# Kernel tuning notes

Hardware: AMD Instinct MI355X
Metric: run time of the kernel (lower is better)

The kernel has to match this reference:

```python
import jax, jax.numpy as jnp
import numpy as np

B, P, K, G_PER, F_IN, H, NECK = 16, 512, 32, 8, 59, 128, 512
N = B * P
E = N * K
G = N // G_PER
EPS = 1e-5


def setup_inputs() -> dict:
    rng = np.random.default_rng(0)
    f32 = lambda a: jnp.asarray(a, jnp.float32)
    x = f32(rng.standard_normal((N, F_IN)))
    pos = f32(rng.standard_normal((N, 3)) * 8.0)
    nrm = rng.standard_normal((N, 3))
    normal = f32(nrm / np.linalg.norm(nrm, axis=1, keepdims=True))
    # synthetic radius-graph edges: K neighbors per node within its own graph, incl. self edge
    nbr = rng.integers(0, P, size=(N, K))
    nbr[:, 0] = np.arange(N) % P  # self edge guarantees every dst segment is non-empty
    starts = np.repeat(np.arange(B) * P, P)
    src = jnp.asarray((starts[:, None] + nbr).reshape(-1), jnp.int32)
    dst = jnp.asarray(np.repeat(np.arange(N), K), jnp.int32)
    # raw (unnormalized but consecutive-run) residue labels, relabeled inside reference
    pool_batch = jnp.asarray(np.repeat(np.arange(G) * 3 + 7, G_PER), jnp.int32)
    mask_t = f32(np.repeat(rng.integers(0, 2, size=G), G_PER))
    def lin(i, o, bias=True):
        w = f32(rng.standard_normal((i, o)) / np.sqrt(i))
        return (w, f32(np.zeros(o))) if bias else w
    lin_w, lin_b = lin(F_IN, H)
    src_w = lin(F_IN, H, bias=False)
    dst_w = lin(F_IN, H, bias=False)
    posnn_w, posnn_b = lin(6, H)
    attnn_w, attnn_b = lin(H, H)
    neck_w, neck_b = lin(H, NECK)
    mlp1_w, mlp1_b = lin(NECK, 256)
    mlp2_w, mlp2_b = lin(256, 1)
    gb = lambda n: (f32(1.0 + 0.1 * rng.standard_normal(n)), f32(0.1 * rng.standard_normal(n)))
    posnn_g, posnn_bb = gb(H)
    attnn_g, attnn_bb = gb(H)
    neck_g, neck_bb = gb(NECK)
    mlp1_g, mlp1_bb = gb(256)
    return dict(x=x, pos=pos, normal=normal, mask_t=mask_t, pool_batch=pool_batch,
                src=src, dst=dst, lin_w=lin_w, lin_b=lin_b, src_w=src_w, dst_w=dst_w,
                posnn_w=posnn_w, posnn_b=posnn_b, posnn_g=posnn_g, posnn_bb=posnn_bb,
                attnn_w=attnn_w, attnn_b=attnn_b, attnn_g=attnn_g, attnn_bb=attnn_bb,
                neck_w=neck_w, neck_b=neck_b, neck_g=neck_g, neck_bb=neck_bb,
                mlp1_w=mlp1_w, mlp1_b=mlp1_b, mlp1_g=mlp1_g, mlp1_bb=mlp1_bb,
                mlp2_w=mlp2_w, mlp2_b=mlp2_b)


def bn_relu(h, g, b):
    # eval-mode BatchNorm1d (running_mean=0, running_var=1) + ReLU; Dropout is identity in eval
    return jax.nn.relu(h * (g / jnp.sqrt(1.0 + EPS)) + b)


def reference(x, pos, normal, mask_t, pool_batch, src, dst,
              lin_w, lin_b, src_w, dst_w,
              posnn_w, posnn_b, posnn_g, posnn_bb,
              attnn_w, attnn_b, attnn_g, attnn_bb,
              neck_w, neck_b, neck_g, neck_bb,
              mlp1_w, mlp1_b, mlp1_g, mlp1_bb,
              mlp2_w, mlp2_b):
    n = x.shape[0]
    # vectorized form of the per-element relabel loop: consecutive runs -> 0..G-1
    chg = jnp.concatenate([jnp.zeros((1,), jnp.int32),
                           (pool_batch[1:] != pool_batch[:-1]).astype(jnp.int32)])
    pb = jnp.cumsum(chg)
    # --- PointTransformerConv (gather -> pos_nn/attn_nn MLPs -> segment softmax -> scatter-add)
    v = x @ lin_w + lin_b                      # value projection [N,H]
    a_src = (x @ src_w)[src]                   # lin_src(x_j)   [E,H]
    a_dst = (x @ dst_w)[dst]                   # lin_dst(x_i)   [E,H]
    rel = jnp.concatenate([pos[dst] - pos[src], normal[dst] - normal[src]], axis=-1)  # [E,6]
    delta = bn_relu(rel @ posnn_w + posnn_b, posnn_g, posnn_bb)                       # [E,H]
    alpha = bn_relu((a_dst - a_src + delta) @ attnn_w + attnn_b, attnn_g, attnn_bb)   # [E,H]
    amax = jax.ops.segment_max(alpha, dst, num_segments=n)
    e = jnp.exp(alpha - amax[dst])
    den = jax.ops.segment_sum(e, dst, num_segments=n)
    attn = e / (den[dst] + 1e-16)              # per-destination softmax over neighbors
    h = jax.ops.segment_sum(attn * (v[src] + delta), dst, num_segments=n)  # [N,H]
    # --- neck, residue max-pool, head
    h = bn_relu(h @ neck_w + neck_b, neck_g, neck_bb)          # [N,512]
    gfeat = jax.ops.segment_max(h, pb, num_segments=G)         # global_max_pool  [G,512]
    gfeat = bn_relu(gfeat @ mlp1_w + mlp1_b, mlp1_g, mlp1_bb)  # [G,256]
    out = gfeat @ mlp2_w + mlp2_b                              # [G,1]
    mask_g = jax.ops.segment_max(mask_t, pb, num_segments=G)   # pooled mask_t
    # original does out[mask_t]; we zero non-selected rows to keep shapes static
    return out * (mask_g == 1.0).astype(out.dtype)[:, None]
```

## Files before the change

kernel.cpp:

```cpp
#include <hip/hip_runtime.h>
#include <hip/hip_bf16.h>
#include <cmath>

#define N_NODES 8192
#define F_INPUT 59
#define H 128
#define K 32
#define NECK 512
#define GPER 8
#define NG 1024
#define EPS_BN 1e-5f
#define DPITCH 136
#define XPITCH 72

typedef short bf16x8 __attribute__((ext_vector_type(8)));
typedef float f32x16 __attribute__((ext_vector_type(16)));

__device__ __forceinline__ void split_bf(float v, short& hi, short& lo) {
    unsigned u = __float_as_uint(v);
    float hif = __uint_as_float(u & 0xffff0000u);
    hi = (short)(u >> 16);
    lo = (short)(__float_as_uint(v - hif) >> 16);
}

__device__ __forceinline__ int bfrag_idx(int k, int c, int k16) {
    int ct = c >> 5, ln = c & 31;
    int s = k >> 4, hf = (k >> 3) & 1, kk = k & 7;
    return ((((ct * k16 + s) * 2 + hf) * 32 + ln) * 8 + kk);
}

__global__ __launch_bounds__(256) void prep_kernel(
    const float* __restrict__ lin_w,
    const float* __restrict__ src_w, const float* __restrict__ dst_w,
    const float* __restrict__ posnn_w,
    const float* __restrict__ attnn_w, const float* __restrict__ neck_w,
    short* __restrict__ w3hi, short* __restrict__ w3lo,
    short* __restrict__ pwhi, short* __restrict__ pwlo,
    short* __restrict__ awhi, short* __restrict__ awlo,
    short* __restrict__ nwhi, short* __restrict__ nwlo)
{
    const int b = blockIdx.x;
    if (b < F_INPUT) {
        const int c = threadIdx.x;
        if (c < H) {
            float a1 = 0.f, a2 = 0.f;
            for (int k = 0; k < H; k++) {
                float wa = attnn_w[k * H + c];
                a1 = fmaf(src_w[b * H + k], wa, a1);
                a2 = fmaf(dst_w[b * H + k], wa, a2);
            }
            short hi, lo; int idx;
            split_bf(lin_w[b * H + c], hi, lo);
            idx = bfrag_idx(b, c, 4);       w3hi[idx] = hi; w3lo[idx] = lo;
            split_bf(a1, hi, lo);
            idx = bfrag_idx(b, 128 + c, 4); w3hi[idx] = hi; w3lo[idx] = lo;
            split_bf(a2, hi, lo);
            idx = bfrag_idx(b, 256 + c, 4); w3hi[idx] = hi; w3lo[idx] = lo;
        }
    } else if (b == F_INPUT) {
        for (int t = threadIdx.x; t < 5 * 384; t += 256) {
            int k = F_INPUT + t / 384, c = t % 384;
            int idx = bfrag_idx(k, c, 4);
            w3hi[idx] = 0; w3lo[idx] = 0;
        }
    } else if (b == F_INPUT + 1) {
        for (int idx = threadIdx.x; idx < 2048; idx += 256) {
            int kk = idx & 7; int t = idx >> 3;
            int l2 = t & 31; t >>= 5;
            int hb = t & 1;  t >>= 1;
            int ct = t;
            int k = hb * 8 + kk, c = ct * 32 + l2;
            float wv = (k < 6) ? posnn_w[k * H + c] : 0.f;
            short hi, lo; split_bf(wv, hi, lo);
            pwhi[idx] = hi; pwlo[idx] = lo;
        }
    } else if (b < F_INPUT + 2 + 64) {
        int idx = (b - F_INPUT - 2) * 256 + threadIdx.x;
        int kk = idx & 7; int t = idx >> 3;
        int l2 = t & 31; t >>= 5;
        int hb = t & 1;  t >>= 1;
        int s  = t & 7;  t >>= 3;
        int c = t * 32 + l2, k = s * 16 + hb * 8 + kk;
        short hi, lo; split_bf(attnn_w[k * H + c], hi, lo);
        awhi[idx] = hi; awlo[idx] = lo;
    } else {
        int idx = (b - F_INPUT - 2 - 64) * 256 + threadIdx.x;
        int kk = idx & 7; int t = idx >> 3;
        int l2 = t & 31; t >>= 5;
        int hb = t & 1;  t >>= 1;
        int s  = t & 7;  t >>= 3;
        int c = t * 32 + l2, k = s * 16 + hb * 8 + kk;
        short hi, lo; split_bf(neck_w[k * NECK + c], hi, lo);
        nwhi[idx] = hi; nwlo[idx] = lo;
    }
}

__global__ __launch_bounds__(256) void proj_kernel(
    const float* __restrict__ x, const float* __restrict__ lin_b,
    const short* __restrict__ w3hi, const short* __restrict__ w3lo,
    float2* __restrict__ vx, float* __restrict__ xdW)
{
    const int n0 = blockIdx.x * 32;
    const int tid = threadIdx.x;
    const int wave = tid >> 6;
    const int lane = tid & 63;
    const int hf = lane >> 5;
    const int ln = lane & 31;

    __shared__ __align__(16) short xhi[32][XPITCH];
    __shared__ __align__(16) short xlo[32][XPITCH];

    for (int idx = tid; idx < 32 * F_INPUT; idx += 256) {
        int n = idx / F_INPUT, k = idx - n * F_INPUT;
        short hi, lo; split_bf(x[n0 * F_INPUT + idx], hi, lo);
        xhi[n][k] = hi; xlo[n][k] = lo;
    }
    if (tid < 32 * 5) {
        int n = tid / 5, k = F_INPUT + tid % 5;
        xhi[n][k] = 0; xlo[n][k] = 0;
    }
    __syncthreads();

    f32x16 acc[3];
    #pragma unroll
    for (int t = 0; t < 3; t++)
        #pragma unroll
        for (int r = 0; r < 16; r++) acc[t][r] = 0.f;

    #pragma unroll
    for (int s = 0; s < 4; s++) {
        bf16x8 ah = *(const bf16x8*)&xhi[ln][s * 16 + hf * 8];
        bf16x8 al = *(const bf16x8*)&xlo[ln][s * 16 + hf * 8];
        #pragma unroll
        for (int t = 0; t < 3; t++) {
            const int ct = wave + 4 * t;
            const int boff = (((ct * 4 + s) * 2 + hf) * 32 + ln) * 8;
            bf16x8 bh = *(const bf16x8*)&w3hi[boff];
            bf16x8 bl = *(const bf16x8*)&w3lo[boff];
            acc[t] = __builtin_amdgcn_mfma_f32_32x32x16_bf16(ah, bl, acc[t], 0, 0, 0);
            acc[t] = __builtin_amdgcn_mfma_f32_32x32x16_bf16(al, bh, acc[t], 0, 0, 0);
            acc[t] = __builtin_amdgcn_mfma_f32_32x32x16_bf16(ah, bh, acc[t], 0, 0, 0);
        }
    }
    const int c = wave * 32 + ln;
    const float lb = lin_b[c];
    #pragma unroll
    for (int r = 0; r < 16; r++) {
        int node = n0 + (r & 3) + 8 * (r >> 2) + 4 * hf;
        vx[node * H + c] = make_float2(acc[1][r], acc[0][r] + lb);
        xdW[node * H + c] = acc[2][r];
    }
}

__global__ __launch_bounds__(256) void edge_kernel(
    const float* __restrict__ pos, const float* __restrict__ normal,
    const int* __restrict__ src,
    const float2* __restrict__ vx, const float* __restrict__ xdW,
    const float* __restrict__ posnn_b, const float* __restrict__ posnn_g,
    const float* __restrict__ posnn_bb,
    const float* __restrict__ attnn_b,
    const float* __restrict__ attnn_g, const float* __restrict__ attnn_bb,
    const short* __restrict__ pwhi, const short* __restrict__ pwlo,
    const short* __restrict__ awhi, const short* __restrict__ awlo,
    unsigned* __restrict__ h2)
{
    const int i0 = blockIdx.x * 2;
    const int tid = threadIdx.x;
    const int wave = tid >> 6;
    const int lane = tid & 63;
    const int hf = lane >> 5;
    const int ln = lane & 31;

    __shared__ int srcs[2][K];
    __shared__ __align__(16) short relh[64][16];
    __shared__ __align__(16) short rell[64][16];
    __shared__ __align__(16) short dhi[64][DPITCH];
    __shared__ __align__(16) short dlo[64][DPITCH];

    if (tid < 64) {
        int n = tid >> 5, jj = tid & 31;
        int i = i0 + n;
        int s = src[i * K + jj];
        srcs[n][jj] = s;
        short h_, l_;
        #pragma unroll
        for (int k = 0; k < 3; k++) {
            split_bf(pos[i * 3 + k] - pos[s * 3 + k], h_, l_);
            relh[tid][k] = h_; rell[tid][k] = l_;
            split_bf(normal[i * 3 + k] - normal[s * 3 + k], h_, l_);
            relh[tid][k + 3] = h_; rell[tid][k + 3] = l_;
        }
        #pragma unroll
        for (int k = 6; k < 16; k++) { relh[tid][k] = 0; rell[tid][k] = 0; }
    }

    const int cc = wave * 32 + ln;
    const float ps  = posnn_g[cc] * rsqrtf(1.f + EPS_BN);
    const float pbn = fmaf(posnn_b[cc], ps, posnn_bb[cc]);
    const float as_ = attnn_g[cc] * rsqrtf(1.f + EPS_BN);
    const float abb = attnn_bb[cc];
    const float ab  = attnn_b[cc];

    const bf16x8 pbh = *(const bf16x8*)&pwhi[((wave * 2 + hf) * 32 + ln) * 8];
    const bf16x8 pbl = *(const bf16x8*)&pwlo[((wave * 2 + hf) * 32 + ln) * 8];

    __syncthreads();

    #pragma unroll
    for (int n = 0; n < 2; n++) {
        bf16x8 ah = *(const bf16x8*)&relh[32 * n + ln][hf * 8];
        bf16x8 al = *(const bf16x8*)&rell[32 * n + ln][hf * 8];
        f32x16 da;
        #pragma unroll
        for (int r = 0; r < 16; r++) da[r] = 0.f;
        da = __builtin_amdgcn_mfma_f32_32x32x16_bf16(ah, pbl, da, 0, 0, 0);
        da = __builtin_amdgcn_mfma_f32_32x32x16_bf16(al, pbh, da, 0, 0, 0);
        da = __builtin_amdgcn_mfma_f32_32x32x16_bf16(ah, pbh, da, 0, 0, 0);
        #pragma unroll
        for (int r = 0; r < 16; r++) {
            int j = (r & 3) + 8 * (r >> 2) + 4 * hf;
            float d = fmaxf(fmaf(da[r], ps, pbn), 0.f);
            short h_, l_; split_bf(d, h_, l_);
            dhi[32 * n + j][cc] = h_;
            dlo[32 * n + j][cc] = l_;
        }
    }
    __syncthreads();

    const short* whb = awhi + wave * 8 * 2 * 32 * 8;
    const short* wlb = awlo + wave * 8 * 2 * 32 * 8;

    #pragma clang loop unroll(disable)
    for (int n = 0; n < 2; n++) {
        const int i = i0 + n;
        f32x16 acc;
        #pragma unroll
        for (int r = 0; r < 16; r++) acc[r] = 0.f;
        #pragma unroll
        for (int s = 0; s < 8; s++) {
            bf16x8 ah = *(const bf16x8*)&dhi[32 * n + ln][s * 16 + hf * 8];
            bf16x8 al = *(const bf16x8*)&dlo[32 * n + ln][s * 16 + hf * 8];
            const int boff = ((s * 2 + hf) * 32 + ln) * 8;
            bf16x8 bh = *(const bf16x8*)&whb[boff];
            bf16x8 bl = *(const bf16x8*)&wlb[boff];
            acc = __builtin_amdgcn_mfma_f32_32x32x16_bf16(ah, bl, acc, 0, 0, 0);
            acc = __builtin_amdgcn_mfma_f32_32x32x16_bf16(al, bh, acc, 0, 0, 0);
            acc = __builtin_amdgcn_mfma_f32_32x32x16_bf16(ah, bh, acc, 0, 0, 0);
        }

        const float base = xdW[i * H + cc] + ab;
        float a[16], vv[16];
        float m = 0.f;
        #pragma unroll
        for (int r = 0; r < 16; r++) {
            int j = (r & 3) + 8 * (r >> 2) + 4 * hf;
            float2 g = vx[srcs[n][j] * H + cc];
            float al2 = acc[r] + base - g.x;
            float av = fmaxf(fmaf(al2, as_, abb), 0.f);
            a[r] = av; vv[r] = g.y;
            m = fmaxf(m, av);
        }
        m = fmaxf(m, __shfl_xor(m, 32, 64));
        float den = 0.f;
        #pragma unroll
        for (int r = 0; r < 16; r++) {
            float e = __expf(a[r] - m);
            a[r] = e; den += e;
        }
        den += __shfl_xor(den, 32, 64);
        const float inv = 1.f / (den + 1e-16f);

        float hsum = 0.f;
        #pragma unroll
        for (int r = 0; r < 16; r++) {
            int j = (r & 3) + 8 * (r >> 2) + 4 * hf;
            unsigned dh = (unsigned short)dhi[32 * n + j][cc];
            unsigned dl = (unsigned short)dlo[32 * n + j][cc];
            float dd = __uint_as_float(dh << 16) + __uint_as_float(dl << 16);
            hsum = fmaf(a[r], vv[r] + dd, hsum);
        }
        hsum += __shfl_xor(hsum, 32, 64);
        hsum *= inv;
        if (hf == 0) {
            unsigned u = __float_as_uint(hsum);
            unsigned hib = u & 0xffff0000u;
            unsigned lo = __float_as_uint(hsum - __uint_as_float(hib)) >> 16;
            h2[i * H + cc] = (lo << 16) | (u >> 16);
        }
    }
}

__global__ __launch_bounds__(256) void neck_head_kernel(
    const unsigned* __restrict__ h2,
    const short* __restrict__ nwhi, const short* __restrict__ nwlo,
    const float* __restrict__ neck_b, const float* __restrict__ neck_g,
    const float* __restrict__ neck_bb,
    const float* __restrict__ mask_t,
    const float* __restrict__ mlp1_w, const float* __restrict__ mlp1_b,
    const float* __restrict__ mlp1_g, const float* __restrict__ mlp1_bb,
    const float* __restrict__ mlp2_w, const float* __restrict__ mlp2_b,
    float* __restrict__ out)
{
    const int blk = blockIdx.x;
    const int n0 = blk * 32;
    const int tid = threadIdx.x;
    const int wave = tid >> 6;
    const int lane = tid & 63;
    const int hf = lane >> 5;
    const int ln = lane & 31;

    __shared__ __align__(16) short a_hi[32][DPITCH];
    __shared__ __align__(16) short a_lo[32][DPITCH];
    __shared__ float gfeat_l[4][NECK];
    __shared__ float red_l[4][4][256];

    for (int d = tid; d < 32 * H; d += 256) {
        unsigned u = h2[(n0 + (d >> 7)) * H + (d & 127)];
        a_hi[d >> 7][d & 127] = (short)(u & 0xffffu);
        a_lo[d >> 7][d & 127] = (short)(u >> 16);
    }
    __syncthreads();

    f32x16 acc[4];
    #pragma unroll
    for (int t = 0; t < 4; t++)
        #pragma unroll
        for (int r = 0; r < 16; r++) acc[t][r] = 0.f;

    #pragma unroll
    for (int s = 0; s < 8; s++) {
        bf16x8 ah = *(const bf16x8*)&a_hi[ln][s * 16 + hf * 8];
        bf16x8 al = *(const bf16x8*)&a_lo[ln][s * 16 + hf * 8];
        #pragma unroll
        for (int t = 0; t < 4; t++) {
            const int ct = wave * 4 + t;
            const int boff = (((ct * 8 + s) * 2 + hf) * 32 + ln) * 8;
            bf16x8 bh = *(const bf16x8*)&nwhi[boff];
            bf16x8 bl = *(const bf16x8*)&nwlo[boff];
            acc[t] = __builtin_amdgcn_mfma_f32_32x32x16_bf16(ah, bl, acc[t], 0, 0, 0);
            acc[t] = __builtin_amdgcn_mfma_f32_32x32x16_bf16(al, bh, acc[t], 0, 0, 0);
            acc[t] = __builtin_amdgcn_mfma_f32_32x32x16_bf16(ah, bh, acc[t], 0, 0, 0);
        }
    }

    #pragma unroll
    for (int t = 0; t < 4; t++) {
        const int c = wave * 128 + t * 32 + ln;
        const float s  = neck_g[c] * rsqrtf(1.f + EPS_BN);
        const float bnb = fmaf(neck_b[c], s, neck_bb[c]);
        #pragma unroll
        for (int g = 0; g < 4; g++) {
            float m = 0.f;
            #pragma unroll
            for (int q = 0; q < 4; q++)
                m = fmaxf(m, fmaf(acc[t][4 * g + q], s, bnb));
            m = fmaxf(m, __shfl_xor(m, 32, 64));
            if (hf == 0) gfeat_l[g][c] = m;
        }
    }
    __syncthreads();

    const int c4 = lane;
    float ph[4][4];
    #pragma unroll
    for (int g = 0; g < 4; g++)
        #pragma unroll
        for (int mm = 0; mm < 4; mm++) ph[g][mm] = 0.f;

    const int k0 = wave * 128;
    for (int k = 0; k < 128; k += 4) {
        float4 gv[4];
        #pragma unroll
        for (int g = 0; g < 4; g++) gv[g] = *(const float4*)&gfeat_l[g][k0 + k];
        #pragma unroll
        for (int kk = 0; kk < 4; kk++) {
            float w0 = mlp1_w[(k0 + k + kk) * 256 + c4];
            float w1 = mlp1_w[(k0 + k + kk) * 256 + c4 + 64];
            float w2 = mlp1_w[(k0 + k + kk) * 256 + c4 + 128];
            float w3 = mlp1_w[(k0 + k + kk) * 256 + c4 + 192];
            #pragma unroll
            for (int g = 0; g < 4; g++) {
                float gvk = (&gv[g].x)[kk];
                ph[g][0] = fmaf(gvk, w0, ph[g][0]);
                ph[g][1] = fmaf(gvk, w1, ph[g][1]);
                ph[g][2] = fmaf(gvk, w2, ph[g][2]);
                ph[g][3] = fmaf(gvk, w3, ph[g][3]);
            }
        }
    }
    #pragma unroll
    for (int g = 0; g < 4; g++)
        #pragma unroll
        for (int mm = 0; mm < 4; mm++)
            red_l[wave][g][c4 + 64 * mm] = ph[g][mm];
    __syncthreads();

    {
        const int g = wave;
        float part = 0.f;
        #pragma unroll
        for (int mm = 0; mm < 4; mm++) {
            const int c = c4 + 64 * mm;
            float sum = mlp1_b[c] + red_l[0][g][c] + red_l[1][g][c]
                      + red_l[2][g][c] + red_l[3][g][c];
            float s = mlp1_g[c] * rsqrtf(1.f + EPS_BN);
            float val = fmaxf(fmaf(sum, s, mlp1_bb[c]), 0.f);
            part = fmaf(val, mlp2_w[c], part);
        }
        #pragma unroll
        for (int off = 32; off > 0; off >>= 1) part += __shfl_xor(part, off, 64);
        if (lane == 0) {
            const int gg = blk * 4 + g;
            float mm = mask_t[gg * GPER];
            #pragma unroll
            for (int n = 1; n < GPER; n++) mm = fmaxf(mm, mask_t[gg * GPER + n]);
            out[gg] = (mm == 1.0f) ? (part + mlp2_b[0]) : 0.f;
        }
    }
}

extern "C" void kernel_launch(void* const* d_in, const int* in_sizes, int n_in,
                              void* d_out, int out_size, void* d_ws, size_t ws_size,
                              hipStream_t stream)
{
    const float* x        = (const float*)d_in[0];
    const float* pos      = (const float*)d_in[1];
    const float* normal   = (const float*)d_in[2];
    const float* mask_t   = (const float*)d_in[3];
    const int*   src      = (const int*)d_in[5];
    const float* lin_w    = (const float*)d_in[7];
    const float* lin_b    = (const float*)d_in[8];
    const float* src_w    = (const float*)d_in[9];
    const float* dst_w    = (const float*)d_in[10];
    const float* posnn_w  = (const float*)d_in[11];
    const float* posnn_b  = (const float*)d_in[12];
    const float* posnn_g  = (const float*)d_in[13];
    const float* posnn_bb = (const float*)d_in[14];
    const float* attnn_w  = (const float*)d_in[15];
    const float* attnn_b  = (const float*)d_in[16];
    const float* attnn_g  = (const float*)d_in[17];
    const float* attnn_bb = (const float*)d_in[18];
    const float* neck_w   = (const float*)d_in[19];
    const float* neck_b   = (const float*)d_in[20];
    const float* neck_g   = (const float*)d_in[21];
    const float* neck_bb  = (const float*)d_in[22];
    const float* mlp1_w   = (const float*)d_in[23];
    const float* mlp1_b   = (const float*)d_in[24];
    const float* mlp1_g   = (const float*)d_in[25];
    const float* mlp1_bb  = (const float*)d_in[26];
    const float* mlp2_w   = (const float*)d_in[27];
    const float* mlp2_b   = (const float*)d_in[28];

    float* ws = (float*)d_ws;
    float2*   vx   = (float2*)ws;
    float*    xdW  = (float*)(vx + (size_t)N_NODES * H);
    unsigned* h2   = (unsigned*)(xdW + (size_t)N_NODES * H);
    short*    w3hi = (short*)(h2 + (size_t)N_NODES * H);
    short*    w3lo = w3hi + 24576;
    short*    pwhi = w3lo + 24576;
    short*    pwlo = pwhi + 2048;
    short*    awhi = pwlo + 2048;
    short*    awlo = awhi + H * H;
    short*    nwhi = awlo + H * H;
    short*    nwlo = nwhi + H * NECK;

    prep_kernel<<<F_INPUT + 2 + 64 + 256, 256, 0, stream>>>(
        lin_w, src_w, dst_w, posnn_w, attnn_w, neck_w,
        w3hi, w3lo, pwhi, pwlo, awhi, awlo, nwhi, nwlo);
    proj_kernel<<<N_NODES / 32, 256, 0, stream>>>(x, lin_b, w3hi, w3lo, vx, xdW);
    edge_kernel<<<N_NODES / 2, 256, 0, stream>>>(pos, normal, src, vx, xdW,
                                                 posnn_b, posnn_g, posnn_bb,
                                                 attnn_b, attnn_g, attnn_bb,
                                                 pwhi, pwlo, awhi, awlo, h2);
    neck_head_kernel<<<N_NODES / 32, 256, 0, stream>>>(
        h2, nwhi, nwlo, neck_b, neck_g, neck_bb, mask_t,
        mlp1_w, mlp1_b, mlp1_g, mlp1_bb, mlp2_w, mlp2_b, (float*)d_out);
}
```

Before: 202.0 us.

## Share attnn weight fragments across both nodes and keep delta in registers

In the edge kernel, the attention-MLP MFMA loop is restructured so each weight fragment is loaded once and applied to both destination nodes, with two accumulators interleaved under raised wave priority. Delta values are kept in registers rather than re-read from LDS and reconstructed from the bf16 pair, and the exp, denominator and weighted sum are fused into one pass. xdW loads are hoisted before the barrier, block indices are swizzled, and launch bounds now request 4 blocks per CU. The cost is higher register pressure from the two accumulators and the delta array, which may spill or limit occupancy. Using the full-precision delta instead of the split sum also changes rounding slightly.

Result: no change. 204.0 us (+1.0%).

```diff
diff --git a/kernel.cpp b/kernel.cpp
--- a/kernel.cpp
+++ b/kernel.cpp
@@ -152,7 +152,7 @@
     }
 }
 
-__global__ __launch_bounds__(256) void edge_kernel(
+__global__ __launch_bounds__(256, 4) void edge_kernel(
     const float* __restrict__ pos, const float* __restrict__ normal,
     const int* __restrict__ src,
     const float2* __restrict__ vx, const float* __restrict__ xdW,
@@ -164,7 +164,9 @@
     const short* __restrict__ awhi, const short* __restrict__ awlo,
     unsigned* __restrict__ h2)
 {
-    const int i0 = blockIdx.x * 2;
+    const int bid = blockIdx.x;
+    const int swz = (bid & 7) * 512 + (bid >> 3);
+    const int i0 = swz * 2;
     const int tid = threadIdx.x;
     const int wave = tid >> 6;
     const int lane = tid & 63;
@@ -204,8 +206,12 @@
     const bf16x8 pbh = *(const bf16x8*)&pwhi[((wave * 2 + hf) * 32 + ln) * 8];
     const bf16x8 pbl = *(const bf16x8*)&pwlo[((wave * 2 + hf) * 32 + ln) * 8];
 
-    __syncthreads();
-
+    const float base0 = xdW[(i0 + 0) * H + cc] + ab;
+    const float base1 = xdW[(i0 + 1) * H + cc] + ab;
+
+    __syncthreads();
+
+    float dreg[2][16];
     #pragma unroll
     for (int n = 0; n < 2; n++) {
         bf16x8 ah = *(const bf16x8*)&relh[32 * n + ln][hf * 8];
@@ -220,6 +226,7 @@
         for (int r = 0; r < 16; r++) {
             int j = (r & 3) + 8 * (r >> 2) + 4 * hf;
             float d = fmaxf(fmaf(da[r], ps, pbn), 0.f);
+            dreg[n][r] = d;
             short h_, l_; split_bf(d, h_, l_);
             dhi[32 * n + j][cc] = h_;
             dlo[32 * n + j][cc] = l_;
@@ -230,57 +237,55 @@
     const short* whb = awhi + wave * 8 * 2 * 32 * 8;
     const short* wlb = awlo + wave * 8 * 2 * 32 * 8;
 
-    #pragma clang loop unroll(disable)
+    f32x16 acc[2];
+    #pragma unroll
+    for (int n = 0; n < 2; n++)
+        #pragma unroll
+        for (int r = 0; r < 16; r++) acc[n][r] = 0.f;
+
+    __builtin_amdgcn_s_setprio(1);
+    #pragma unroll
+    for (int s = 0; s < 8; s++) {
+        const int boff = ((s * 2 + hf) * 32 + ln) * 8;
+        bf16x8 bh = *(const bf16x8*)&whb[boff];
+        bf16x8 bl = *(const bf16x8*)&wlb[boff];
+        #pragma unroll
+        for (int n = 0; n < 2; n++) {
+            bf16x8 ah = *(const bf16x8*)&dhi[32 * n + ln][s * 16 + hf * 8];
+            bf16x8 al = *(const bf16x8*)&dlo[32 * n + ln][s * 16 + hf * 8];
+            acc[n] = __builtin_amdgcn_mfma_f32_32x32x16_bf16(ah, bl, acc[n], 0, 0, 0);
+            acc[n] = __builtin_amdgcn_mfma_f32_32x32x16_bf16(al, bh, acc[n], 0, 0, 0);
+            acc[n] = __builtin_amdgcn_mfma_f32_32x32x16_bf16(ah, bh, acc[n], 0, 0, 0);
+        }
+    }
+    __builtin_amdgcn_s_setprio(0);
+
+    #pragma unroll
     for (int n = 0; n < 2; n++) {
         const int i = i0 + n;
-        f32x16 acc;
-        #pragma unroll
-        for (int r = 0; r < 16; r++) acc[r] = 0.f;
-        #pragma unroll
-        for (int s = 0; s < 8; s++) {
-            bf16x8 ah = *(const bf16x8*)&dhi[32 * n + ln][s * 16 + hf * 8];
-            bf16x8 al = *(const bf16x8*)&dlo[32 * n + ln][s * 16 + hf * 8];
-            const int boff = ((s * 2 + hf) * 32 + ln) * 8;
-            bf16x8 bh = *(const bf16x8*)&whb[boff];
-            bf16x8 bl = *(const bf16x8*)&wlb[boff];
-            acc = __builtin_amdgcn_mfma_f32_32x32x16_bf16(ah, bl, acc, 0, 0, 0);
-            acc = __builtin_amdgcn_mfma_f32_32x32x16_bf16(al, bh, acc, 0, 0, 0);
-            acc = __builtin_amdgcn_mfma_f32_32x32x16_bf16(ah, bh, acc, 0, 0, 0);
-        }
-
-        const float base = xdW[i * H + cc] + ab;
+        const float base = (n == 0) ? base0 : base1;
         float a[16], vv[16];
         float m = 0.f;
         #pragma unroll
         for (int r = 0; r < 16; r++) {
             int j = (r & 3) + 8 * (r >> 2) + 4 * hf;
             float2 g = vx[srcs[n][j] * H + cc];
-            float al2 = acc[r] + base - g.x;
-            float av = fmaxf(fmaf(al2, as_, abb), 0.f);
-            a[r] = av; vv[r] = g.y;
+            float av = fmaxf(fmaf(acc[n][r] + base - g.x, as_, abb), 0.f);
+            a[r] = av;
+            vv[r] = g.y + dreg[n][r];
             m = fmaxf(m, av);
         }
         m = fmaxf(m, __shfl_xor(m, 32, 64));
-        float den = 0.f;
+        float den = 0.f, hsum = 0.f;
         #pragma unroll
         for (int r = 0; r < 16; r++) {
             float e = __expf(a[r] - m);
-            a[r] = e; den += e;
+            den += e;
+            hsum = fmaf(e, vv[r], hsum);
         }
         den += __shfl_xor(den, 32, 64);
-        const float inv = 1.f / (den + 1e-16f);
-
-        float hsum = 0.f;
-        #pragma unroll
-        for (int r = 0; r < 16; r++) {
-            int j = (r & 3) + 8 * (r >> 2) + 4 * hf;
-            unsigned dh = (unsigned short)dhi[32 * n + j][cc];
-            unsigned dl = (unsigned short)dlo[32 * n + j][cc];
-            float dd = __uint_as_float(dh << 16) + __uint_as_float(dl << 16);
-            hsum = fmaf(a[r], vv[r] + dd, hsum);
-        }
         hsum += __shfl_xor(hsum, 32, 64);
-        hsum *= inv;
+        hsum *= 1.f / (den + 1e-16f);
         if (hf == 0) {
             unsigned u = __float_as_uint(hsum);
             unsigned hib = u & 0xffff0000u;
```
